# Kernel optimization log

Measured on AMD Instinct MI355X. Metric: run time of the kernel, lower is better.

The kernel has to match this reference:

```python
import math
import jax, jax.numpy as jnp
import numpy as np

B, C, H, W = 2, 256, 128, 128
C8 = C // 8
MAX_TOKENS = 4096
S = int(math.isqrt(MAX_TOKENS))  # 64; H,W divisible by S -> exact 2x2 mean pool


def setup_inputs() -> dict:
    key = jax.random.key(0)
    ks = jax.random.split(key, 8)
    sc = 1.0 / math.sqrt(C)
    return {
        "x": jax.random.normal(ks[0], (B, C, H, W), dtype=jnp.float32),
        "Wq": jax.random.normal(ks[1], (C8, C), dtype=jnp.float32) * sc,
        "bq": jax.random.normal(ks[2], (C8,), dtype=jnp.float32) * 0.01,
        "Wk": jax.random.normal(ks[3], (C8, C), dtype=jnp.float32) * sc,
        "bk": jax.random.normal(ks[4], (C8,), dtype=jnp.float32) * 0.01,
        "Wv": jax.random.normal(ks[5], (C, C), dtype=jnp.float32) * sc,
        "bv": jax.random.normal(ks[6], (C,), dtype=jnp.float32) * 0.01,
        # torch inits gamma to 0; use small nonzero so the attention path is exercised
        "gamma": jax.random.normal(ks[7], (1,), dtype=jnp.float32) * 0.1,
    }


def _pool_to_s(t):
    # adaptive_avg_pool2d to (S,S); exact since H%S==0, W%S==0
    b, ch, h, w = t.shape
    return t.reshape(b, ch, S, h // S, S, w // S).mean(axis=(3, 5))


def reference(x, Wq, bq, Wk, bk, Wv, bv, gamma):
    b, c, h, w = x.shape
    # 1x1 convs as channel contractions
    q = jnp.einsum('bchw,oc->bohw', x, Wq) + bq[None, :, None, None]   # (b,c8,h,w)
    k = jnp.einsum('bchw,oc->bohw', x, Wk) + bk[None, :, None, None]   # (b,c8,h,w)
    v = jnp.einsum('bchw,oc->bohw', x, Wv) + bv[None, :, None, None]   # (b,c,h,w)

    q = q.reshape(b, C8, h * w).transpose(0, 2, 1)                      # (b, hw, c8)
    if h * w > MAX_TOKENS:
        k = _pool_to_s(k)
        v = _pool_to_s(v)
    k = k.reshape(b, C8, -1)                                            # (b, c8, s2)
    v = v.reshape(b, c, -1)                                             # (b, c, s2)

    attn = jnp.einsum('btc,bcs->bts', q, k) / math.sqrt(k.shape[1])     # (b, hw, s2)
    attn = jax.nn.softmax(attn, axis=-1)
    out = jnp.einsum('bcs,bts->bct', v, attn).reshape(b, c, h, w)
    return gamma[0] * out + x
```

## Files before the change

### kernel.cpp

```cpp
#include <hip/hip_runtime.h>

typedef unsigned short u16;
typedef unsigned int u32;
typedef unsigned long long u64;
typedef float f32x4 __attribute__((ext_vector_type(4)));
typedef __bf16 bf16x8 __attribute__((ext_vector_type(8)));

__device__ __forceinline__ u16 f2bf(float f) {
  unsigned u = __float_as_uint(f);
  unsigned r = u + 0x7fffu + ((u >> 16) & 1u);
  return (u16)(r >> 16);
}
__device__ __forceinline__ u32 cvt_pk_bf16(float lo, float hi) {
  u32 r;
  asm("v_cvt_pk_bf16_f32 %0, %1, %2" : "=v"(r) : "v"(lo), "v"(hi));
  return r;
}
__device__ __forceinline__ float exp2_hw(float x) {
  float r;
  asm("v_exp_f32 %0, %1" : "=v"(r) : "v"(x));
  return r;
}
__device__ __forceinline__ bf16x8 f32x8_to_bf16x8(float4 a, float4 b) {
  union { u32 u[4]; bf16x8 v; } t;
  t.u[0] = cvt_pk_bf16(a.x, a.y);
  t.u[1] = cvt_pk_bf16(a.z, a.w);
  t.u[2] = cvt_pk_bf16(b.x, b.y);
  t.u[3] = cvt_pk_bf16(b.z, b.w);
  return t.v;
}
__device__ __forceinline__ void gload_lds16(const void* g, u16* l) {
  __builtin_amdgcn_global_load_lds(
      (const __attribute__((address_space(1))) unsigned int*)g,
      (__attribute__((address_space(3))) unsigned int*)l, 16, 0, 0);
}

#define QSCALE 0.25513936f

__global__ __launch_bounds__(256) void proj_kernel(
    const float* __restrict__ x, const float* __restrict__ Wq, const float* __restrict__ bq,
    const float* __restrict__ Wk, const float* __restrict__ bk, const float* __restrict__ Wv,
    const float* __restrict__ bv, u16* __restrict__ Qb, u16* __restrict__ Kt,
    u16* __restrict__ Vb) {
  __shared__ __align__(16) u16 smem[24576];
  const int tid = threadIdx.x;
  const int lane = tid & 63, w = tid >> 6;
  const int l15 = lane & 15, l4 = lane >> 4;
  const int bi = blockIdx.x;
  const f32x4 zero = {0.f, 0.f, 0.f, 0.f};

  if (bi >= 256) {
    u16* xt = smem;
    u16* wq = smem + 16384;
    const int j = bi - 256;
    const int b = j >> 8, tb = j & 255;
    const float* xp = x + (size_t)b * 256 * 16384 + tb * 64;

    for (int i = tid; i < 4096; i += 256) {
      int oc = i >> 7, c0 = (i & 127) * 2;
      float2 f = *reinterpret_cast<const float2*>(Wq + oc * 256 + c0);
      u32 pk = cvt_pk_bf16(f.x * QSCALE, f.y * QSCALE);
      *reinterpret_cast<u32*>((char*)wq + oc * 512 + (((c0 >> 3) ^ (oc & 7)) * 16) +
                              (c0 & 7) * 2) = pk;
    }
#pragma unroll
    for (int rr = 0; rr < 4; ++rr) {
      int c = rr * 64 + (tid >> 2);
      int tch = (tid & 3) * 16;
      const float* src = xp + (size_t)c * 16384 + tch;
#pragma unroll
      for (int u = 0; u < 4; ++u) {
        float4 f = *reinterpret_cast<const float4*>(src + u * 4);
        int t = tch + u * 4;
        *reinterpret_cast<u16*>((char*)xt + (t + 0) * 512 + (((c >> 3) ^ ((t + 0) & 7)) * 16) + (c & 7) * 2) = f2bf(f.x);
        *reinterpret_cast<u16*>((char*)xt + (t + 1) * 512 + (((c >> 3) ^ ((t + 1) & 7)) * 16) + (c & 7) * 2) = f2bf(f.y);
        *reinterpret_cast<u16*>((char*)xt + (t + 2) * 512 + (((c >> 3) ^ ((t + 2) & 7)) * 16) + (c & 7) * 2) = f2bf(f.z);
        *reinterpret_cast<u16*>((char*)xt + (t + 3) * 512 + (((c >> 3) ^ ((t + 3) & 7)) * 16) + (c & 7) * 2) = f2bf(f.w);
      }
    }
    __syncthreads();

    f32x4 acc[2] = {zero, zero};
    const int tl = w * 16 + l15;
#pragma unroll
    for (int k = 0; k < 8; ++k) {
      bf16x8 bf = *reinterpret_cast<const bf16x8*>((char*)xt + tl * 512 +
                                                   (((k * 4 + l4) ^ (tl & 7)) * 16));
#pragma unroll
      for (int m = 0; m < 2; ++m) {
        int oc = m * 16 + l15;
        bf16x8 af = *reinterpret_cast<const bf16x8*>((char*)wq + oc * 512 +
                                                     (((k * 4 + l4) ^ (oc & 7)) * 16));
        acc[m] = __builtin_amdgcn_mfma_f32_16x16x32_bf16(af, bf, acc[m], 0, 0, 0);
      }
    }
    const int t = tb * 64 + tl;
#pragma unroll
    for (int m = 0; m < 2; ++m) {
      int oc0 = m * 16 + l4 * 4;
      u32 p0 = cvt_pk_bf16(acc[m][0] + bq[oc0] * QSCALE, acc[m][1] + bq[oc0 + 1] * QSCALE);
      u32 p1 = cvt_pk_bf16(acc[m][2] + bq[oc0 + 2] * QSCALE, acc[m][3] + bq[oc0 + 3] * QSCALE);
      u16* dst = Qb + ((size_t)b * 16384 + t) * 32 + oc0;
      *reinterpret_cast<u32*>(dst) = p0;
      *reinterpret_cast<u32*>(dst + 2) = p1;
    }
  } else {
    u16* xs = smem;
    const int b = bi >> 7, r2 = bi & 127;
    const int sy = r2 >> 1, z = r2 & 1;
    const int mb = z * 8;
    const float* xb = x + (size_t)b * 256 * 16384;

#pragma unroll
    for (int rr = 0; rr < 4; ++rr) {
      int c = rr * 64 + (tid >> 2);
      int f4base = (tid & 3) * 8;
      const float* r0 = xb + (size_t)c * 16384 + (size_t)sy * 256;
#pragma unroll
      for (int u = 0; u < 8; ++u) {
        int jj = f4base + u;
        float4 a = *reinterpret_cast<const float4*>(r0 + jj * 4);
        float4 d = *reinterpret_cast<const float4*>(r0 + 128 + jj * 4);
        float p0 = (a.x + a.y + d.x + d.y) * 0.25f;
        float p1 = (a.z + a.w + d.z + d.w) * 0.25f;
        int s0 = jj * 2;
        *reinterpret_cast<u16*>((char*)xs + (s0 + 0) * 512 + (((c >> 3) ^ ((s0 + 0) & 7)) * 16) + (c & 7) * 2) = f2bf(p0);
        *reinterpret_cast<u16*>((char*)xs + (s0 + 1) * 512 + (((c >> 3) ^ ((s0 + 1) & 7)) * 16) + (c & 7) * 2) = f2bf(p1);
      }
    }
    __syncthreads();

    f32x4 acc[10];
#pragma unroll
    for (int m = 0; m < 10; ++m) acc[m] = zero;
    const int sl = w * 16 + l15;
#pragma unroll
    for (int k = 0; k < 8; ++k) {
      bf16x8 bf = *reinterpret_cast<const bf16x8*>((char*)xs + sl * 512 +
                                                   (((k * 4 + l4) ^ (sl & 7)) * 16));
      if (z == 0) {
#pragma unroll
        for (int m = 0; m < 2; ++m) {
          const float* wr = Wk + (size_t)(m * 16 + l15) * 256 + k * 32 + l4 * 8;
          float4 fa = *reinterpret_cast<const float4*>(wr);
          float4 fb = *reinterpret_cast<const float4*>(wr + 4);
          acc[m] = __builtin_amdgcn_mfma_f32_16x16x32_bf16(f32x8_to_bf16x8(fa, fb), bf, acc[m], 0, 0, 0);
        }
      }
#pragma unroll
      for (int mm = 0; mm < 8; ++mm) {
        const float* wr = Wv + (size_t)((mb + mm) * 16 + l15) * 256 + k * 32 + l4 * 8;
        float4 fa = *reinterpret_cast<const float4*>(wr);
        float4 fb = *reinterpret_cast<const float4*>(wr + 4);
        acc[2 + mm] = __builtin_amdgcn_mfma_f32_16x16x32_bf16(f32x8_to_bf16x8(fa, fb), bf, acc[2 + mm], 0, 0, 0);
      }
    }
    if (z == 0) {
#pragma unroll
      for (int m = 0; m < 2; ++m) {
        int oc0 = m * 16 + l4 * 4;
        u32 p0 = cvt_pk_bf16(acc[m][0] + bk[oc0], acc[m][1] + bk[oc0 + 1]);
        u32 p1 = cvt_pk_bf16(acc[m][2] + bk[oc0 + 2], acc[m][3] + bk[oc0 + 3]);
        u16* dst = Kt + ((size_t)b * 4096 + sy * 64 + sl) * 32 + oc0;
        *reinterpret_cast<u32*>(dst) = p0;
        *reinterpret_cast<u32*>(dst + 2) = p1;
      }
    }
#pragma unroll
    for (int mm = 0; mm < 8; ++mm) {
#pragma unroll
      for (int r = 0; r < 4; ++r) {
        int oc = (mb + mm) * 16 + l4 * 4 + r;
        Vb[((size_t)b * 256 + oc) * 4096 + sy * 64 + sl] = f2bf(acc[2 + mm][r] + bv[oc]);
      }
    }
  }
}

__global__ __launch_bounds__(256, 2) void attn_kernel(
    const u16* __restrict__ Qb, const u16* __restrict__ Kt, const u16* __restrict__ Vb,
    const float* __restrict__ x, const float* __restrict__ gamma, float* __restrict__ out) {
  __shared__ __align__(16) u16 p_lds[2][128 * 64];
  __shared__ __align__(16) u16 v_lds[2][128 * 64];

  const int tid = threadIdx.x;
  const int lane = tid & 63, w = tid >> 6;
  const int l15 = lane & 15, l4 = lane >> 4, l7 = l15 & 7;
  const int raw = blockIdx.x;
  const int xcd = raw & 7, loc = raw >> 3;
  const int b = xcd >> 2;
  const int H = loc & 1;
  const int tt = (xcd & 3) * 32 + (loc >> 1);
  const int t0 = tt * 128;
  const int th = w >> 1, chh = w & 1;
  const int CHW = H * 128 + chh * 64;

  const u16* Qp = Qb + (size_t)(b * 16384 + t0) * 32;
  const u16* Kp = Kt + (size_t)b * 4096 * 32;
  const char* Kpc = (const char*)Kp;
  const char* Vpc = (const char*)(Vb + (size_t)b * 256 * 4096);

  bf16x8 qfr[8];
#pragma unroll
  for (int mt = 0; mt < 8; ++mt)
    qfr[mt] = *reinterpret_cast<const bf16x8*>(Qp + (size_t)(mt * 16 + l15) * 32 + l4 * 8);

  const int key = w * 16 + l15;
  const int pw_chunk = w * 2 + (l4 >> 1), pw_off = (l4 & 1) * 8;

  char* pA0 = (char*)p_lds + (th * 64 + l15) * 128 + ((l4 ^ l7) * 16);
  char* pA1 = (char*)p_lds + (th * 64 + l15) * 128 + (((4 + l4) ^ l7) * 16);
  char* pW = (char*)p_lds + l15 * 128 + ((pw_chunk ^ l7) * 16) + pw_off;
  char* pV0 = (char*)v_lds + chh * 8192 + (l15 >> 3) * 1024 + l7 * 128 + ((l4 ^ l7) * 16);
  char* pV1 = (char*)v_lds + chh * 8192 + (l15 >> 3) * 1024 + l7 * 128 + (((4 ^ l4) ^ l7) * 16);

  const int sch = lane >> 3;
  const int skc = (lane & 7) ^ sch;
  u32 vstg = (u32)(H * 128 + w * 32 + sch) * 8192 + (u32)skc * 16 + 128;
  u32 vok = 2 * 4096 + key * 64 + l4 * 16;

  f32x4 acc[4][4] = {};
  float lsum[8] = {};
  const f32x4 zero = {0.f, 0.f, 0.f, 0.f};

#pragma unroll
  for (int i = 0; i < 4; ++i)
    gload_lds16(Vpc + (vstg - 128) + i * 65536, (u16*)v_lds + (w * 4 + i) * 512);
  {
    bf16x8 k0 = *reinterpret_cast<const bf16x8*>(Kp + (size_t)key * 32 + l4 * 8);
#pragma unroll
    for (int mt = 0; mt < 8; ++mt) {
      f32x4 s = __builtin_amdgcn_mfma_f32_16x16x32_bf16(k0, qfr[mt], zero, 0, 0, 0);
      float p0 = exp2_hw(fminf(s[0], 28.f)), p1 = exp2_hw(fminf(s[1], 28.f));
      float p2 = exp2_hw(fminf(s[2], 28.f)), p3 = exp2_hw(fminf(s[3], 28.f));
      lsum[mt] += (p0 + p1) + (p2 + p3);
      *reinterpret_cast<u64*>(pW + mt * 2048) =
          (u64)cvt_pk_bf16(p0, p1) | ((u64)cvt_pk_bf16(p2, p3) << 32);
    }
  }
  bf16x8 kfr = *reinterpret_cast<const bf16x8*>(Kpc + (4096 + key * 64 + l4 * 16));
  __syncthreads();

#define ATTN_ITER(KT, CUR)                                                               \
  {                                                                                      \
    if ((KT) < 63) {                                                                     \
             \
      _Pragma("unroll") for (int i = 0; i < 4; ++i)                                      \
          gload_lds16(Vpc + vstg + i * 65536,                                            \
                      (u16*)v_lds + ((CUR) ^ 1) * 8192 + (w * 4 + i) * 512);             \
      vstg += 128;                                                                       \
    }                                                                                    \
                             \
    bf16x8 afr0[4], vfr0[4];                                                             \
    _Pragma("unroll") for (int mt = 0; mt < 4; ++mt)                                     \
        afr0[mt] = *reinterpret_cast<const bf16x8*>(pA0 + ((CUR)*16384 + mt * 2048));    \
    _Pragma("unroll") for (int nt = 0; nt < 4; ++nt)                                     \
        vfr0[nt] = *reinterpret_cast<const bf16x8*>(pV0 + ((CUR)*16384 + nt * 2048));    \
    if ((KT) < 63) {                                                                     \
                                         \
      _Pragma("unroll") for (int mt = 0; mt < 8; ++mt) {                                 \
        f32x4 s = __builtin_amdgcn_mfma_f32_16x16x32_bf16(kfr, qfr[mt], zero, 0, 0, 0);  \
        float p0 = exp2_hw(fminf(s[0], 28.f)), p1 = exp2_hw(fminf(s[1], 28.f));          \
        float p2 = exp2_hw(fminf(s[2], 28.f)), p3 = exp2_hw(fminf(s[3], 28.f));          \
        lsum[mt] += (p0 + p1) + (p2 + p3);                                               \
        *reinterpret_cast<u64*>(pW + (((CUR) ^ 1) * 16384 + mt * 2048)) =                \
            (u64)cvt_pk_bf16(p0, p1) | ((u64)cvt_pk_bf16(p2, p3) << 32);                 \
      }                                                                                  \
      if ((KT) < 62) {                                                                   \
        kfr = *reinterpret_cast<const bf16x8*>(Kpc + vok);                               \
        vok += 4096;                                                                     \
      }                                                                                  \
    }                                                                                    \
                                \
    __builtin_amdgcn_s_setprio(1);                                                       \
    _Pragma("unroll") for (int mt = 0; mt < 4; ++mt)                                     \
      _Pragma("unroll") for (int nt = 0; nt < 4; ++nt)                                   \
        acc[mt][nt] =                                                                    \
            __builtin_amdgcn_mfma_f32_16x16x32_bf16(afr0[mt], vfr0[nt], acc[mt][nt], 0, 0, 0); \
    bf16x8 afr1[4], vfr1[4];                                                             \
    _Pragma("unroll") for (int mt = 0; mt < 4; ++mt)                                     \
        afr1[mt] = *reinterpret_cast<const bf16x8*>(pA1 + ((CUR)*16384 + mt * 2048));    \
    _Pragma("unroll") for (int nt = 0; nt < 4; ++nt)                                     \
        vfr1[nt] = *reinterpret_cast<const bf16x8*>(pV1 + ((CUR)*16384 + nt * 2048));    \
    _Pragma("unroll") for (int mt = 0; mt < 4; ++mt)                                     \
      _Pragma("unroll") for (int nt = 0; nt < 4; ++nt)                                   \
        acc[mt][nt] =                                                                    \
            __builtin_amdgcn_mfma_f32_16x16x32_bf16(afr1[mt], vfr1[nt], acc[mt][nt], 0, 0, 0); \
    __builtin_amdgcn_s_setprio(0);                                                       \
    __syncthreads();                                                                     \
  }

  for (int it = 0; it < 32; ++it) {
    ATTN_ITER(2 * it, 0)
    ATTN_ITER(2 * it + 1, 1)
  }
#undef ATTN_ITER

  float* lred = (float*)v_lds;
#pragma unroll
  for (int mt = 0; mt < 8; ++mt) {
    lsum[mt] += __shfl_xor(lsum[mt], 16, 64);
    lsum[mt] += __shfl_xor(lsum[mt], 32, 64);
  }
  if (l4 == 0) {
#pragma unroll
    for (int mt = 0; mt < 8; ++mt) lred[w * 128 + mt * 16 + l15] = lsum[mt];
  }
  __syncthreads();

  const float g = gamma[0];
  float linv[16];
#pragma unroll
  for (int mt = 0; mt < 4; ++mt)
#pragma unroll
    for (int r = 0; r < 4; ++r) {
      int tok = th * 64 + mt * 16 + l4 * 4 + r;
      linv[mt * 4 + r] =
          1.0f / (lred[tok] + lred[128 + tok] + lred[256 + tok] + lred[384 + tok]);
    }
#pragma unroll
  for (int mt = 0; mt < 4; ++mt) {
#pragma unroll
    for (int nt = 0; nt < 4; ++nt) {
      int ch = CHW + nt * 16 + l15;
      size_t idx = ((size_t)(b * 256 + ch)) * 16384 + t0 + th * 64 + mt * 16 + l4 * 4;
      float4 xr = *reinterpret_cast<const float4*>(x + idx);
      float4 o;
      o.x = g * acc[mt][nt][0] * linv[mt * 4 + 0] + xr.x;
      o.y = g * acc[mt][nt][1] * linv[mt * 4 + 1] + xr.y;
      o.z = g * acc[mt][nt][2] * linv[mt * 4 + 2] + xr.z;
      o.w = g * acc[mt][nt][3] * linv[mt * 4 + 3] + xr.w;
      *reinterpret_cast<float4*>(out + idx) = o;
    }
  }
}

extern "C" void kernel_launch(void* const* d_in, const int* in_sizes, int n_in,
                              void* d_out, int out_size, void* d_ws, size_t ws_size,
                              hipStream_t stream) {
  const float* x = (const float*)d_in[0];
  const float* Wq = (const float*)d_in[1];
  const float* bq = (const float*)d_in[2];
  const float* Wk = (const float*)d_in[3];
  const float* bk = (const float*)d_in[4];
  const float* Wv = (const float*)d_in[5];
  const float* bv = (const float*)d_in[6];
  const float* gamma = (const float*)d_in[7];
  float* out = (float*)d_out;

  char* ws = (char*)d_ws;
  u16* Qb = (u16*)ws;
  u16* Kt = (u16*)(ws + (2u << 20));
  u16* Vb = (u16*)(ws + (2u << 20) + (512u << 10));

  proj_kernel<<<dim3(768), 256, 0, stream>>>(x, Wq, bq, Wk, bk, Wv, bv, Qb, Kt, Vb);
  attn_kernel<<<dim3(512), 256, 0, stream>>>(Qb, Kt, Vb, x, gamma, out);
}
```

Before: 137.5 us.

## Restructure attention blocks to 64 tokens × all channels with 8 waves

Each attention block now covers 64 tokens and all 256 channels with 512 threads, where it previously covered 128 tokens and half the channels with 256 threads. Each exp(QK) score is therefore computed once per token per block, so the duplicated score work across the two channel halves disappears. V is single-buffered in LDS and P is double-buffered. The P writes and the V prefetch move after a barrier, which adds a second __syncthreads per key tile. The intent is to remove redundant softmax and exp work and raise occupancy, at the cost of more synchronisation and less overlap between the V load and the MFMAs.

```diff
diff --git a/kernel.cpp b/kernel.cpp
--- a/kernel.cpp
+++ b/kernel.cpp
@@ -177,11 +177,11 @@
   }
 }
 
-__global__ __launch_bounds__(256, 2) void attn_kernel(
+__global__ __launch_bounds__(512, 4) void attn_kernel(
     const u16* __restrict__ Qb, const u16* __restrict__ Kt, const u16* __restrict__ Vb,
     const float* __restrict__ x, const float* __restrict__ gamma, float* __restrict__ out) {
-  __shared__ __align__(16) u16 p_lds[2][128 * 64];
-  __shared__ __align__(16) u16 v_lds[2][128 * 64];
+  __shared__ __align__(16) u16 p_lds[2][64 * 64];
+  __shared__ __align__(16) u16 v_lds[256 * 64];
 
   const int tid = threadIdx.x;
   const int lane = tid & 63, w = tid >> 6;
@@ -189,47 +189,47 @@
   const int raw = blockIdx.x;
   const int xcd = raw & 7, loc = raw >> 3;
   const int b = xcd >> 2;
-  const int H = loc & 1;
-  const int tt = (xcd & 3) * 32 + (loc >> 1);
-  const int t0 = tt * 128;
-  const int th = w >> 1, chh = w & 1;
-  const int CHW = H * 128 + chh * 64;
+  const int tt = (xcd & 3) * 64 + loc;
+  const int t0 = tt * 64;
+  const int kw = w & 3, thf = w >> 2;
+  const int chq = w & 3;
 
   const u16* Qp = Qb + (size_t)(b * 16384 + t0) * 32;
   const u16* Kp = Kt + (size_t)b * 4096 * 32;
   const char* Kpc = (const char*)Kp;
   const char* Vpc = (const char*)(Vb + (size_t)b * 256 * 4096);
 
-  bf16x8 qfr[8];
-#pragma unroll
-  for (int mt = 0; mt < 8; ++mt)
-    qfr[mt] = *reinterpret_cast<const bf16x8*>(Qp + (size_t)(mt * 16 + l15) * 32 + l4 * 8);
-
-  const int key = w * 16 + l15;
-  const int pw_chunk = w * 2 + (l4 >> 1), pw_off = (l4 & 1) * 8;
-
-  char* pA0 = (char*)p_lds + (th * 64 + l15) * 128 + ((l4 ^ l7) * 16);
-  char* pA1 = (char*)p_lds + (th * 64 + l15) * 128 + (((4 + l4) ^ l7) * 16);
-  char* pW = (char*)p_lds + l15 * 128 + ((pw_chunk ^ l7) * 16) + pw_off;
-  char* pV0 = (char*)v_lds + chh * 8192 + (l15 >> 3) * 1024 + l7 * 128 + ((l4 ^ l7) * 16);
-  char* pV1 = (char*)v_lds + chh * 8192 + (l15 >> 3) * 1024 + l7 * 128 + (((4 ^ l4) ^ l7) * 16);
+  bf16x8 qfr[2];
+#pragma unroll
+  for (int mt = 0; mt < 2; ++mt)
+    qfr[mt] = *reinterpret_cast<const bf16x8*>(Qp + (size_t)(thf * 32 + mt * 16 + l15) * 32 + l4 * 8);
+
+  const int key = kw * 16 + l15;
+  const int pw_chunk = kw * 2 + (l4 >> 1), pw_off = (l4 & 1) * 8;
+
+  char* pA0 = (char*)p_lds + (thf * 32 + l15) * 128 + ((l4 ^ l7) * 16);
+  char* pA1 = (char*)p_lds + (thf * 32 + l15) * 128 + (((4 ^ l4) ^ l7) * 16);
+  char* pW = (char*)p_lds + (thf * 32 + l15) * 128 + ((pw_chunk ^ l7) * 16) + pw_off;
+  char* pV0 = (char*)v_lds + (chq * 64 + l15) * 128 + ((l4 ^ l7) * 16);
+  char* pV1 = (char*)v_lds + (chq * 64 + l15) * 128 + (((4 ^ l4) ^ l7) * 16);
 
   const int sch = lane >> 3;
   const int skc = (lane & 7) ^ sch;
-  u32 vstg = (u32)(H * 128 + w * 32 + sch) * 8192 + (u32)skc * 16 + 128;
-  u32 vok = 2 * 4096 + key * 64 + l4 * 16;
-
-  f32x4 acc[4][4] = {};
-  float lsum[8] = {};
+  const u32 vstg0 = (u32)(w * 32 + sch) * 8192 + (u32)skc * 16;
+  u32 vstg = vstg0 + 128;
+  u32 vok = 2 * 4096 + (u32)key * 64 + l4 * 16;
+
+  f32x4 acc[2][4] = {};
+  float lsum[2] = {};
   const f32x4 zero = {0.f, 0.f, 0.f, 0.f};
 
 #pragma unroll
   for (int i = 0; i < 4; ++i)
-    gload_lds16(Vpc + (vstg - 128) + i * 65536, (u16*)v_lds + (w * 4 + i) * 512);
+    gload_lds16(Vpc + vstg0 + i * 65536, (u16*)v_lds + (w * 4 + i) * 512);
   {
-    bf16x8 k0 = *reinterpret_cast<const bf16x8*>(Kp + (size_t)key * 32 + l4 * 8);
-#pragma unroll
-    for (int mt = 0; mt < 8; ++mt) {
+    bf16x8 k0 = *reinterpret_cast<const bf16x8*>(Kpc + (size_t)key * 64 + l4 * 16);
+#pragma unroll
+    for (int mt = 0; mt < 2; ++mt) {
       f32x4 s = __builtin_amdgcn_mfma_f32_16x16x32_bf16(k0, qfr[mt], zero, 0, 0, 0);
       float p0 = exp2_hw(fminf(s[0], 28.f)), p1 = exp2_hw(fminf(s[1], 28.f));
       float p2 = exp2_hw(fminf(s[2], 28.f)), p3 = exp2_hw(fminf(s[3], 28.f));
@@ -238,92 +238,96 @@
           (u64)cvt_pk_bf16(p0, p1) | ((u64)cvt_pk_bf16(p2, p3) << 32);
     }
   }
-  bf16x8 kfr = *reinterpret_cast<const bf16x8*>(Kpc + (4096 + key * 64 + l4 * 16));
+  bf16x8 kfrA = *reinterpret_cast<const bf16x8*>(Kpc + (4096 + (size_t)key * 64 + l4 * 16));
+  bf16x8 kfrB;
   __syncthreads();
 
-#define ATTN_ITER(KT, CUR)                                                               \
-  {                                                                                      \
-    if ((KT) < 63) {                                                                     \
-             \
-      _Pragma("unroll") for (int i = 0; i < 4; ++i)                                      \
-          gload_lds16(Vpc + vstg + i * 65536,                                            \
-                      (u16*)v_lds + ((CUR) ^ 1) * 8192 + (w * 4 + i) * 512);             \
-      vstg += 128;                                                                       \
-    }                                                                                    \
-                             \
-    bf16x8 afr0[4], vfr0[4];                                                             \
-    _Pragma("unroll") for (int mt = 0; mt < 4; ++mt)                                     \
-        afr0[mt] = *reinterpret_cast<const bf16x8*>(pA0 + ((CUR)*16384 + mt * 2048));    \
-    _Pragma("unroll") for (int nt = 0; nt < 4; ++nt)                                     \
-        vfr0[nt] = *reinterpret_cast<const bf16x8*>(pV0 + ((CUR)*16384 + nt * 2048));    \
-    if ((KT) < 63) {                                                                     \
-                                         \
-      _Pragma("unroll") for (int mt = 0; mt < 8; ++mt) {                                 \
-        f32x4 s = __builtin_amdgcn_mfma_f32_16x16x32_bf16(kfr, qfr[mt], zero, 0, 0, 0);  \
-        float p0 = exp2_hw(fminf(s[0], 28.f)), p1 = exp2_hw(fminf(s[1], 28.f));          \
-        float p2 = exp2_hw(fminf(s[2], 28.f)), p3 = exp2_hw(fminf(s[3], 28.f));          \
-        lsum[mt] += (p0 + p1) + (p2 + p3);                                               \
-        *reinterpret_cast<u64*>(pW + (((CUR) ^ 1) * 16384 + mt * 2048)) =                \
-            (u64)cvt_pk_bf16(p0, p1) | ((u64)cvt_pk_bf16(p2, p3) << 32);                 \
-      }                                                                                  \
-      if ((KT) < 62) {                                                                   \
-        kfr = *reinterpret_cast<const bf16x8*>(Kpc + vok);                               \
-        vok += 4096;                                                                     \
-      }                                                                                  \
-    }                                                                                    \
-                                \
-    __builtin_amdgcn_s_setprio(1);                                                       \
-    _Pragma("unroll") for (int mt = 0; mt < 4; ++mt)                                     \
-      _Pragma("unroll") for (int nt = 0; nt < 4; ++nt)                                   \
-        acc[mt][nt] =                                                                    \
+#define ATTN_ITER(KT, CUR, KC, KN)                                                        \
+  {                                                                                       \
+                            \
+    if ((KT) < 62) { KN = *reinterpret_cast<const bf16x8*>(Kpc + vok); vok += 4096; }     \
+                                      \
+    bf16x8 afr0[2], vfr0[4];                                                              \
+    _Pragma("unroll") for (int mt = 0; mt < 2; ++mt)                                      \
+        afr0[mt] = *reinterpret_cast<const bf16x8*>(pA0 + ((CUR)*8192 + mt * 2048));      \
+    _Pragma("unroll") for (int nt = 0; nt < 4; ++nt)                                      \
+        vfr0[nt] = *reinterpret_cast<const bf16x8*>(pV0 + nt * 2048);                     \
+                                  \
+    u64 pk0 = 0, pk1 = 0;                                                                 \
+    if ((KT) < 63) {                                                                      \
+      f32x4 s0 = __builtin_amdgcn_mfma_f32_16x16x32_bf16(KC, qfr[0], zero, 0, 0, 0);      \
+      f32x4 s1 = __builtin_amdgcn_mfma_f32_16x16x32_bf16(KC, qfr[1], zero, 0, 0, 0);      \
+      float a0 = exp2_hw(fminf(s0[0], 28.f)), a1 = exp2_hw(fminf(s0[1], 28.f));           \
+      float a2 = exp2_hw(fminf(s0[2], 28.f)), a3 = exp2_hw(fminf(s0[3], 28.f));           \
+      float b0 = exp2_hw(fminf(s1[0], 28.f)), b1 = exp2_hw(fminf(s1[1], 28.f));           \
+      float b2 = exp2_hw(fminf(s1[2], 28.f)), b3 = exp2_hw(fminf(s1[3], 28.f));           \
+      lsum[0] += (a0 + a1) + (a2 + a3);                                                   \
+      lsum[1] += (b0 + b1) + (b2 + b3);                                                   \
+      pk0 = (u64)cvt_pk_bf16(a0, a1) | ((u64)cvt_pk_bf16(a2, a3) << 32);                  \
+      pk1 = (u64)cvt_pk_bf16(b0, b1) | ((u64)cvt_pk_bf16(b2, b3) << 32);                  \
+    }                                                                                     \
+                                                               \
+    __builtin_amdgcn_s_setprio(1);                                                        \
+    _Pragma("unroll") for (int mt = 0; mt < 2; ++mt)                                      \
+      _Pragma("unroll") for (int nt = 0; nt < 4; ++nt)                                    \
+        acc[mt][nt] =                                                                     \
             __builtin_amdgcn_mfma_f32_16x16x32_bf16(afr0[mt], vfr0[nt], acc[mt][nt], 0, 0, 0); \
-    bf16x8 afr1[4], vfr1[4];                                                             \
-    _Pragma("unroll") for (int mt = 0; mt < 4; ++mt)                                     \
-        afr1[mt] = *reinterpret_cast<const bf16x8*>(pA1 + ((CUR)*16384 + mt * 2048));    \
-    _Pragma("unroll") for (int nt = 0; nt < 4; ++nt)                                     \
-        vfr1[nt] = *reinterpret_cast<const bf16x8*>(pV1 + ((CUR)*16384 + nt * 2048));    \
-    _Pragma("unroll") for (int mt = 0; mt < 4; ++mt)                                     \
-      _Pragma("unroll") for (int nt = 0; nt < 4; ++nt)                                   \
-        acc[mt][nt] =                                                                    \
+    bf16x8 afr1[2], vfr1[4];                                                              \
+    _Pragma("unroll") for (int mt = 0; mt < 2; ++mt)                                      \
+        afr1[mt] = *reinterpret_cast<const bf16x8*>(pA1 + ((CUR)*8192 + mt * 2048));      \
+    _Pragma("unroll") for (int nt = 0; nt < 4; ++nt)                                      \
+        vfr1[nt] = *reinterpret_cast<const bf16x8*>(pV1 + nt * 2048);                     \
+    _Pragma("unroll") for (int mt = 0; mt < 2; ++mt)                                      \
+      _Pragma("unroll") for (int nt = 0; nt < 4; ++nt)                                    \
+        acc[mt][nt] =                                                                     \
             __builtin_amdgcn_mfma_f32_16x16x32_bf16(afr1[mt], vfr1[nt], acc[mt][nt], 0, 0, 0); \
-    __builtin_amdgcn_s_setprio(0);                                                       \
-    __syncthreads();                                                                     \
+    __builtin_amdgcn_s_setprio(0);                                                        \
+    __syncthreads();                    \
+                    \
+    if ((KT) < 63) {                                                                      \
+      _Pragma("unroll") for (int i = 0; i < 4; ++i)                                       \
+          gload_lds16(Vpc + vstg + i * 65536, (u16*)v_lds + (w * 4 + i) * 512);           \
+      vstg += 128;                                                                        \
+      *reinterpret_cast<u64*>(pW + (((CUR) ^ 1) * 8192)) = pk0;                           \
+      *reinterpret_cast<u64*>(pW + (((CUR) ^ 1) * 8192 + 2048)) = pk1;                    \
+    }                                                                                     \
+    __syncthreads();                              \
   }
 
   for (int it = 0; it < 32; ++it) {
-    ATTN_ITER(2 * it, 0)
-    ATTN_ITER(2 * it + 1, 1)
+    ATTN_ITER(2 * it, 0, kfrA, kfrB)
+    ATTN_ITER(2 * it + 1, 1, kfrB, kfrA)
   }
 #undef ATTN_ITER
 
   float* lred = (float*)v_lds;
 #pragma unroll
-  for (int mt = 0; mt < 8; ++mt) {
+  for (int mt = 0; mt < 2; ++mt) {
     lsum[mt] += __shfl_xor(lsum[mt], 16, 64);
     lsum[mt] += __shfl_xor(lsum[mt], 32, 64);
   }
   if (l4 == 0) {
 #pragma unroll
-    for (int mt = 0; mt < 8; ++mt) lred[w * 128 + mt * 16 + l15] = lsum[mt];
+    for (int mt = 0; mt < 2; ++mt) lred[kw * 64 + thf * 32 + mt * 16 + l15] = lsum[mt];
   }
   __syncthreads();
 
   const float g = gamma[0];
-  float linv[16];
-#pragma unroll
-  for (int mt = 0; mt < 4; ++mt)
+  float linv[8];
+#pragma unroll
+  for (int mt = 0; mt < 2; ++mt)
 #pragma unroll
     for (int r = 0; r < 4; ++r) {
-      int tok = th * 64 + mt * 16 + l4 * 4 + r;
+      int tok = thf * 32 + mt * 16 + l4 * 4 + r;
       linv[mt * 4 + r] =
-          1.0f / (lred[tok] + lred[128 + tok] + lred[256 + tok] + lred[384 + tok]);
-    }
-#pragma unroll
-  for (int mt = 0; mt < 4; ++mt) {
+          1.0f / (lred[tok] + lred[64 + tok] + lred[128 + tok] + lred[192 + tok]);
+    }
+#pragma unroll
+  for (int mt = 0; mt < 2; ++mt) {
 #pragma unroll
     for (int nt = 0; nt < 4; ++nt) {
-      int ch = CHW + nt * 16 + l15;
-      size_t idx = ((size_t)(b * 256 + ch)) * 16384 + t0 + th * 64 + mt * 16 + l4 * 4;
+      int ch = chq * 64 + nt * 16 + l15;
+      size_t idx = ((size_t)(b * 256 + ch)) * 16384 + t0 + thf * 32 + mt * 16 + l4 * 4;
       float4 xr = *reinterpret_cast<const float4*>(x + idx);
       float4 o;
       o.x = g * acc[mt][nt][0] * linv[mt * 4 + 0] + xr.x;
@@ -354,5 +358,5 @@
   u16* Vb = (u16*)(ws + (2u << 20) + (512u << 10));
 
   proj_kernel<<<dim3(768), 256, 0, stream>>>(x, Wq, bq, Wk, bk, Wv, bv, Qb, Kt, Vb);
-  attn_kernel<<<dim3(512), 256, 0, stream>>>(Qb, Kt, Vb, x, gamma, out);
-}
+  attn_kernel<<<dim3(512), 512, 0, stream>>>(Qb, Kt, Vb, x, gamma, out);
+}
```

Result: faster. 133.5 us (-3.0%).
